# Kernel optimization log

Hardware: AMD Instinct MI355X
Metric: run time of the kernel (lower is better)

## Reference

```python
import jax, jax.numpy as jnp
import numpy as np

B = 262144
IN, H = 2, 50


def setup_inputs() -> dict:
    key = jax.random.key(0)
    ks = jax.random.split(key, 12)
    k = 1.0 / np.sqrt(H)
    u = lambda kk, shape: jax.random.uniform(kk, shape, jnp.float32, -k, k)
    return {
        "s": jax.random.normal(ks[0], (B, IN), jnp.float32),
        "h": jax.random.normal(ks[1], (B, H), jnp.float32),
        "w_ih": u(ks[2], (3 * H, IN)),
        "w_hh": u(ks[3], (3 * H, H)),
        "b_ih": u(ks[4], (3 * H,)),
        "b_hh": u(ks[5], (3 * H,)),
        "actor_w": u(ks[6], (2, H)),
        "actor_b": u(ks[7], (2,)),
        "critic_w": u(ks[8], (1, H)),
        "critic_b": u(ks[9], (1,)),
    }


def reference(s, h, w_ih, w_hh, b_ih, b_hh, actor_w, actor_b, critic_w, critic_b):
    # PyTorch GRUCell gate math (gate order: reset, update, new)
    gi = s @ w_ih.T + b_ih          # [B, 3H]
    gh = h @ w_hh.T + b_hh          # [B, 3H]
    i_r, i_z, i_n = jnp.split(gi, 3, axis=1)
    h_r, h_z, h_n = jnp.split(gh, 3, axis=1)
    r = jax.nn.sigmoid(i_r + h_r)
    z = jax.nn.sigmoid(i_z + h_z)
    n = jnp.tanh(i_n + r * h_n)
    h_new = (1.0 - z) * n + z * h   # [B, H]
    c = h_new @ critic_w.T + critic_b            # [B, 1]
    pi = jax.nn.softmax(h_new @ actor_w.T + actor_b, axis=1)  # [B, 2]
    return h_new, c, pi
```

## Files before the change

kernel.cpp:

```cpp
#include <hip/hip_runtime.h>


#define BDIM 256

typedef __bf16 bf16x8 __attribute__((ext_vector_type(8)));
typedef float f32x4 __attribute__((ext_vector_type(4)));

__device__ __forceinline__ unsigned short f2bf(float f) {
    union { float f; unsigned u; } x; x.f = f;
    unsigned r = x.u + 0x7fffu + ((x.u >> 16) & 1u);
    return (unsigned short)(r >> 16);
}

__global__ __launch_bounds__(BDIM) void gru_fused(
    const float* __restrict__ s,
    const float* __restrict__ h,
    const float* __restrict__ w_ih,
    const float* __restrict__ w_hh,
    const float* __restrict__ b_ih,
    const float* __restrict__ b_hh,
    const float* __restrict__ actor_w,
    const float* __restrict__ actor_b,
    const float* __restrict__ critic_w,
    const float* __restrict__ critic_b,
    float* __restrict__ out,
    int Btot, int nTiles)
{
    __shared__ __align__(16) unsigned short xlds[64 * 72];
    __shared__ __align__(16) unsigned short wlds[1536 * 8];
    __shared__ float hlds[64 * 53];
    __shared__ float sflds[64 * 2];
    __shared__ float awc[150];
    __shared__ float win0l[64], win1l[64], binl[64];

    const int tid  = threadIdx.x;
    const int wave = tid >> 6;
    const int lane = tid & 63;
    const int c16  = lane & 15;
    const int quad = lane >> 4;

    for (int e = tid; e < 1536; e += BDIM) {
        int ln = e & 63;
        int ks = (e >> 6) & 1;
        int t  = (e >> 7) & 3;
        int g  = e >> 9;
        int n  = t * 16 + (ln & 15);
        int kbase = ks * 32 + (ln >> 4) * 8;
        unsigned short vals[8];
        if (n < 50) {
            int r = g * 50 + n;
            #pragma unroll
            for (int i = 0; i < 8; ++i) {
                int k = kbase + i;
                float v = 0.f;
                if (k < 50)       v = w_hh[r * 50 + k];
                else if (k == 50) v = (g < 2) ? w_ih[r * 2 + 0] : 0.f;
                else if (k == 51) v = (g < 2) ? w_ih[r * 2 + 1] : 0.f;
                else if (k == 52) {
                    v = b_hh[r];
                    if (g < 2) v += b_ih[r];
                }
                vals[i] = f2bf(v);
            }
        } else {
            #pragma unroll
            for (int i = 0; i < 8; ++i) vals[i] = 0;
        }
        #pragma unroll
        for (int i = 0; i < 8; ++i) wlds[e * 8 + i] = vals[i];
    }
    for (int k = tid; k < 50; k += BDIM) {
        awc[k]       = actor_w[k];
        awc[50 + k]  = actor_w[50 + k];
        awc[100 + k] = critic_w[k];
    }
    if (tid < 64) {
        int j = tid;
        float w0 = 0.f, w1 = 0.f, bb = 0.f;
        if (j < 50) {
            w0 = w_ih[(100 + j) * 2 + 0];
            w1 = w_ih[(100 + j) * 2 + 1];
            bb = b_ih[100 + j];
        }
        win0l[j] = w0; win1l[j] = w1; binl[j] = bb;
    }

    union U { unsigned short u[8]; bf16x8 v; };
    U aI, bN, bK;
    #pragma unroll
    for (int i = 0; i < 8; ++i) {
        int k = quad * 8 + i;
        aI.u[i] = (k == c16) ? (unsigned short)0x3F80 : (unsigned short)0;
        bN.u[i] = (k < 16) ? f2bf((float)c16) : (unsigned short)0;
        bK.u[i] = (k < 16) ? f2bf((float)k)   : (unsigned short)0;
    }
    f32x4 d1 = {0.f, 0.f, 0.f, 0.f}, d2 = {0.f, 0.f, 0.f, 0.f};
    d1 = __builtin_amdgcn_mfma_f32_16x16x32_bf16(aI.v, bN.v, d1, 0, 0, 0);
    d2 = __builtin_amdgcn_mfma_f32_16x16x32_bf16(aI.v, bK.v, d2, 0, 0, 0);
    int colmap[4], rowmap[4];
    #pragma unroll
    for (int r = 0; r < 4; ++r) {
        colmap[r] = ((int)(d1[r] + 0.5f)) & 15;
        rowmap[r] = ((int)(d2[r] + 0.5f)) & 15;
    }

    const float2* h2 = (const float2*)h;
    const float2* s2 = (const float2*)s;
    unsigned* xlds32 = (unsigned*)xlds;
    float2* out2 = (float2*)out;
    const long long outc_off   = (long long)Btot * 50;
    const long long outpi2_off = ((long long)Btot * 51) >> 1;

    __syncthreads();

    for (int bt = blockIdx.x; bt < nTiles; bt += gridDim.x) {
        const int rowbase = bt * 64;

        for (int d = tid; d < 1600; d += BDIM) {
            int r = d / 25, dk = d - r * 25;
            float2 v = h2[rowbase * 25 + d];
            xlds32[r * 36 + dk] = (unsigned)f2bf(v.x) | ((unsigned)f2bf(v.y) << 16);
            hlds[r * 53 + 2 * dk]     = v.x;
            hlds[r * 53 + 2 * dk + 1] = v.y;
        }
        if (tid < 64) {
            float2 sv = s2[rowbase + tid];
            sflds[tid * 2 + 0] = sv.x;
            sflds[tid * 2 + 1] = sv.y;
            xlds32[tid * 36 + 25] = (unsigned)f2bf(sv.x) | ((unsigned)f2bf(sv.y) << 16);
            xlds32[tid * 36 + 26] = 0x00003f80u;
            #pragma unroll
            for (int q = 27; q < 32; ++q) xlds32[tid * 36 + q] = 0u;
        }
        __syncthreads();

        const unsigned short* arow = &xlds[(wave * 16 + c16) * 72 + quad * 8];
        bf16x8 a0 = *(const bf16x8*)(arow);
        bf16x8 a1 = *(const bf16x8*)(arow + 32);
        f32x4 acc[3][4];
        #pragma unroll
        for (int g = 0; g < 3; ++g) {
            #pragma unroll
            for (int t = 0; t < 4; ++t) {
                f32x4 a = {0.f, 0.f, 0.f, 0.f};
                const unsigned short* wb = &wlds[(((g * 4 + t) * 2) * 64 + lane) * 8];
                bf16x8 b0 = *(const bf16x8*)(wb);
                bf16x8 b1 = *(const bf16x8*)(wb + 64 * 8);
                a = __builtin_amdgcn_mfma_f32_16x16x32_bf16(a0, b0, a, 0, 0, 0);
                a = __builtin_amdgcn_mfma_f32_16x16x32_bf16(a1, b1, a, 0, 0, 0);
                acc[g][t] = a;
            }
        }

        #pragma unroll
        for (int reg = 0; reg < 4; ++reg) {
            int lr = wave * 16 + rowmap[reg];
            float s0 = sflds[lr * 2 + 0];
            float s1 = sflds[lr * 2 + 1];
            int cl = colmap[reg];
            #pragma unroll
            for (int t = 0; t < 4; ++t) {
                int j = t * 16 + cl;
                float pr = acc[0][t][reg];
                float pz = acc[1][t][reg];
                float hn = acc[2][t][reg];
                float inn = fmaf(s1, win1l[j], fmaf(s0, win0l[j], binl[j]));
                float rg = __builtin_amdgcn_rcpf(1.f + __expf(-pr));
                float zg = __builtin_amdgcn_rcpf(1.f + __expf(-pz));
                float x = inn + rg * hn;
                x = fminf(fmaxf(x, -20.f), 20.f);
                float e2 = __expf(2.f * x);
                float ng = (e2 - 1.f) * __builtin_amdgcn_rcpf(e2 + 1.f);
                if (j < 50) {
                    float hv = hlds[lr * 53 + j];
                    hlds[lr * 53 + j] = (1.f - zg) * ng + zg * hv;
                }
            }
        }
        __syncthreads();

        for (int d = tid; d < 1600; d += BDIM) {
            int r = d / 25, dk = d - r * 25;
            float2 v;
            v.x = hlds[r * 53 + 2 * dk];
            v.y = hlds[r * 53 + 2 * dk + 1];
            out2[rowbase * 25 + d] = v;
        }
        if (tid < 64) {
            int gr = rowbase + tid;
            float a0f = actor_b[0], a1f = actor_b[1], cc = critic_b[0];
            #pragma unroll 10
            for (int k = 0; k < 50; ++k) {
                float hv = hlds[tid * 53 + k];
                a0f = fmaf(hv, awc[k], a0f);
                a1f = fmaf(hv, awc[50 + k], a1f);
                cc  = fmaf(hv, awc[100 + k], cc);
            }
            out[outc_off + gr] = cc;
            float m = fmaxf(a0f, a1f);
            float e0 = __expf(a0f - m), e1 = __expf(a1f - m);
            float inv = 1.f / (e0 + e1);
            float2 pv; pv.x = e0 * inv; pv.y = e1 * inv;
            out2[outpi2_off + gr] = pv;
        }
        __syncthreads();
    }
}

extern "C" void kernel_launch(void* const* d_in, const int* in_sizes, int n_in,
                              void* d_out, int out_size, void* d_ws, size_t ws_size,
                              hipStream_t stream) {
    const float* s        = (const float*)d_in[0];
    const float* h        = (const float*)d_in[1];
    const float* w_ih     = (const float*)d_in[2];
    const float* w_hh     = (const float*)d_in[3];
    const float* b_ih     = (const float*)d_in[4];
    const float* b_hh     = (const float*)d_in[5];
    const float* actor_w  = (const float*)d_in[6];
    const float* actor_b  = (const float*)d_in[7];
    const float* critic_w = (const float*)d_in[8];
    const float* critic_b = (const float*)d_in[9];
    float* out = (float*)d_out;

    int Btot = in_sizes[1] / 50;
    int nTiles = Btot / 64;
    int grid = nTiles < 1024 ? nTiles : 1024;

    gru_fused<<<grid, BDIM, 0, stream>>>(s, h, w_ih, w_hh, b_ih, b_hh,
                                         actor_w, actor_b, critic_w, critic_b,
                                         out, Btot, nTiles);
}
```

Measured before the change: 173.9 us.

## Prefetch next tile into registers, drop fp32 h staging, parallelize head

Loads the next tile's h and s into registers while the current tile's MFMA and gate math run, overlapping global loads with compute. The fp32 hlds buffer is removed: h_new is written directly to global memory from the gate loop, and the bf16 copy in xlds is reused for the z*h term and the actor/critic heads. The head dot products are spread across all 256 threads with shuffle reductions instead of 64 threads, the MFMA-probed row/column maps are replaced by the hardcoded layout, and launch bounds request 4 blocks per CU. The risk is accuracy: the z*h blend and the heads now read bf16-rounded h instead of fp32, and the direct per-element output stores are scattered rather than coalesced float2 writes.

```diff
diff --git a/kernel.cpp b/kernel.cpp
--- a/kernel.cpp
+++ b/kernel.cpp
@@ -6,13 +6,19 @@
 typedef __bf16 bf16x8 __attribute__((ext_vector_type(8)));
 typedef float f32x4 __attribute__((ext_vector_type(4)));
 
+__device__ __forceinline__ float bf2f(unsigned short u) {
+    union { unsigned u; float f; } x; x.u = ((unsigned)u) << 16; return x.f;
+}
 __device__ __forceinline__ unsigned short f2bf(float f) {
     union { float f; unsigned u; } x; x.f = f;
     unsigned r = x.u + 0x7fffu + ((x.u >> 16) & 1u);
     return (unsigned short)(r >> 16);
 }
-
-__global__ __launch_bounds__(BDIM) void gru_fused(
+__device__ __forceinline__ unsigned packbf(float a, float b) {
+    return (unsigned)f2bf(a) | ((unsigned)f2bf(b) << 16);
+}
+
+__global__ __launch_bounds__(BDIM, 4) void gru_fused(
     const float* __restrict__ s,
     const float* __restrict__ h,
     const float* __restrict__ w_ih,
@@ -28,9 +34,8 @@
 {
     __shared__ __align__(16) unsigned short xlds[64 * 72];
     __shared__ __align__(16) unsigned short wlds[1536 * 8];
-    __shared__ float hlds[64 * 53];
     __shared__ float sflds[64 * 2];
-    __shared__ float awc[150];
+    __shared__ float awc[152];
     __shared__ float win0l[64], win1l[64], binl[64];
 
     const int tid  = threadIdx.x;
@@ -69,10 +74,11 @@
         #pragma unroll
         for (int i = 0; i < 8; ++i) wlds[e * 8 + i] = vals[i];
     }
-    for (int k = tid; k < 50; k += BDIM) {
-        awc[k]       = actor_w[k];
-        awc[50 + k]  = actor_w[50 + k];
-        awc[100 + k] = critic_w[k];
+    for (int k = tid; k < 152; k += BDIM) {
+        float v = 0.f;
+        if (k < 100)      v = actor_w[k];
+        else if (k < 150) v = critic_w[k - 100];
+        awc[k] = v;
     }
     if (tid < 64) {
         int j = tid;
@@ -84,25 +90,7 @@
         }
         win0l[j] = w0; win1l[j] = w1; binl[j] = bb;
     }
-
-    union U { unsigned short u[8]; bf16x8 v; };
-    U aI, bN, bK;
-    #pragma unroll
-    for (int i = 0; i < 8; ++i) {
-        int k = quad * 8 + i;
-        aI.u[i] = (k == c16) ? (unsigned short)0x3F80 : (unsigned short)0;
-        bN.u[i] = (k < 16) ? f2bf((float)c16) : (unsigned short)0;
-        bK.u[i] = (k < 16) ? f2bf((float)k)   : (unsigned short)0;
-    }
-    f32x4 d1 = {0.f, 0.f, 0.f, 0.f}, d2 = {0.f, 0.f, 0.f, 0.f};
-    d1 = __builtin_amdgcn_mfma_f32_16x16x32_bf16(aI.v, bN.v, d1, 0, 0, 0);
-    d2 = __builtin_amdgcn_mfma_f32_16x16x32_bf16(aI.v, bK.v, d2, 0, 0, 0);
-    int colmap[4], rowmap[4];
-    #pragma unroll
-    for (int r = 0; r < 4; ++r) {
-        colmap[r] = ((int)(d1[r] + 0.5f)) & 15;
-        rowmap[r] = ((int)(d2[r] + 0.5f)) & 15;
-    }
+    const float ab0 = actor_b[0], ab1 = actor_b[1], cb = critic_b[0];
 
     const float2* h2 = (const float2*)h;
     const float2* s2 = (const float2*)s;
@@ -111,28 +99,52 @@
     const long long outc_off   = (long long)Btot * 50;
     const long long outpi2_off = ((long long)Btot * 51) >> 1;
 
-    __syncthreads();
-
-    for (int bt = blockIdx.x; bt < nTiles; bt += gridDim.x) {
+    float2 pf[7];
+    int bt = blockIdx.x;
+    {
+        int rb = bt * 64;
+        #pragma unroll
+        for (int j = 0; j < 7; ++j) {
+            int d = tid + j * 256;
+            if (d < 1600)       pf[j] = h2[rb * 25 + d];
+            else if (d < 1664)  pf[j] = s2[rb + (d - 1600)];
+        }
+    }
+
+    while (bt < nTiles) {
         const int rowbase = bt * 64;
-
-        for (int d = tid; d < 1600; d += BDIM) {
-            int r = d / 25, dk = d - r * 25;
-            float2 v = h2[rowbase * 25 + d];
-            xlds32[r * 36 + dk] = (unsigned)f2bf(v.x) | ((unsigned)f2bf(v.y) << 16);
-            hlds[r * 53 + 2 * dk]     = v.x;
-            hlds[r * 53 + 2 * dk + 1] = v.y;
+        __syncthreads();
+        #pragma unroll
+        for (int j = 0; j < 7; ++j) {
+            int d = tid + j * 256;
+            if (d < 1600) {
+                int r = d / 25, dk = d - r * 25;
+                xlds32[r * 36 + dk] = packbf(pf[j].x, pf[j].y);
+            } else if (d < 1664) {
+                int r = d - 1600;
+                sflds[r * 2 + 0] = pf[j].x;
+                sflds[r * 2 + 1] = pf[j].y;
+                xlds32[r * 36 + 25] = packbf(pf[j].x, pf[j].y);
+            }
         }
         if (tid < 64) {
-            float2 sv = s2[rowbase + tid];
-            sflds[tid * 2 + 0] = sv.x;
-            sflds[tid * 2 + 1] = sv.y;
-            xlds32[tid * 36 + 25] = (unsigned)f2bf(sv.x) | ((unsigned)f2bf(sv.y) << 16);
             xlds32[tid * 36 + 26] = 0x00003f80u;
             #pragma unroll
             for (int q = 27; q < 32; ++q) xlds32[tid * 36 + q] = 0u;
         }
         __syncthreads();
+
+        const int nbt = bt + gridDim.x;
+        {
+            int pb = (nbt < nTiles) ? nbt : bt;
+            int rb = pb * 64;
+            #pragma unroll
+            for (int j = 0; j < 7; ++j) {
+                int d = tid + j * 256;
+                if (d < 1600)       pf[j] = h2[rb * 25 + d];
+                else if (d < 1664)  pf[j] = s2[rb + (d - 1600)];
+            }
+        }
 
         const unsigned short* arow = &xlds[(wave * 16 + c16) * 72 + quad * 8];
         bf16x8 a0 = *(const bf16x8*)(arow);
@@ -154,13 +166,12 @@
 
         #pragma unroll
         for (int reg = 0; reg < 4; ++reg) {
-            int lr = wave * 16 + rowmap[reg];
+            int lr = wave * 16 + quad * 4 + reg;
             float s0 = sflds[lr * 2 + 0];
             float s1 = sflds[lr * 2 + 1];
-            int cl = colmap[reg];
             #pragma unroll
             for (int t = 0; t < 4; ++t) {
-                int j = t * 16 + cl;
+                int j = t * 16 + c16;
                 float pr = acc[0][t][reg];
                 float pz = acc[1][t][reg];
                 float hn = acc[2][t][reg];
@@ -172,38 +183,43 @@
                 float e2 = __expf(2.f * x);
                 float ng = (e2 - 1.f) * __builtin_amdgcn_rcpf(e2 + 1.f);
                 if (j < 50) {
-                    float hv = hlds[lr * 53 + j];
-                    hlds[lr * 53 + j] = (1.f - zg) * ng + zg * hv;
+                    float hv = bf2f(xlds[lr * 72 + j]);
+                    float hnew = (1.f - zg) * ng + zg * hv;
+                    out[(long long)(rowbase + lr) * 50 + j] = hnew;
+                    xlds[lr * 72 + j] = f2bf(hnew);
                 }
             }
         }
         __syncthreads();
 
-        for (int d = tid; d < 1600; d += BDIM) {
-            int r = d / 25, dk = d - r * 25;
-            float2 v;
-            v.x = hlds[r * 53 + 2 * dk];
-            v.y = hlds[r * 53 + 2 * dk + 1];
-            out2[rowbase * 25 + d] = v;
-        }
-        if (tid < 64) {
-            int gr = rowbase + tid;
-            float a0f = actor_b[0], a1f = actor_b[1], cc = critic_b[0];
-            #pragma unroll 10
-            for (int k = 0; k < 50; ++k) {
-                float hv = hlds[tid * 53 + k];
-                a0f = fmaf(hv, awc[k], a0f);
-                a1f = fmaf(hv, awc[50 + k], a1f);
-                cc  = fmaf(hv, awc[100 + k], cc);
-            }
-            out[outc_off + gr] = cc;
-            float m = fmaxf(a0f, a1f);
-            float e0 = __expf(a0f - m), e1 = __expf(a1f - m);
-            float inv = 1.f / (e0 + e1);
-            float2 pv; pv.x = e0 * inv; pv.y = e1 * inv;
-            out2[outpi2_off + gr] = pv;
-        }
-        __syncthreads();
+        {
+            int row = wave * 16 + (lane >> 2);
+            int sub = lane & 3;
+            int kn = (sub == 3) ? 11 : 13;
+            float a0p = 0.f, a1p = 0.f, ccp = 0.f;
+            #pragma unroll
+            for (int i = 0; i < 13; ++i) {
+                int k = sub * 13 + i;
+                float hv = (i < kn) ? bf2f(xlds[row * 72 + k]) : 0.f;
+                a0p = fmaf(hv, awc[k],       a0p);
+                a1p = fmaf(hv, awc[50 + k],  a1p);
+                ccp = fmaf(hv, awc[100 + k], ccp);
+            }
+            a0p += __shfl_xor(a0p, 1); a0p += __shfl_xor(a0p, 2);
+            a1p += __shfl_xor(a1p, 1); a1p += __shfl_xor(a1p, 2);
+            ccp += __shfl_xor(ccp, 1); ccp += __shfl_xor(ccp, 2);
+            if (sub == 0) {
+                int gr = rowbase + row;
+                float A0 = a0p + ab0, A1 = a1p + ab1;
+                out[outc_off + gr] = ccp + cb;
+                float m = fmaxf(A0, A1);
+                float e0 = __expf(A0 - m), e1 = __expf(A1 - m);
+                float inv = 1.f / (e0 + e1);
+                float2 pv; pv.x = e0 * inv; pv.y = e1 * inv;
+                out2[outpi2_off + gr] = pv;
+            }
+        }
+        bt = nbt;
     }
 }
 
```

After: 143.4 us. -17.6%, faster.
